# Kernel tuning notes

Hardware: AMD Instinct MI355X
Metric: run time of the kernel (lower is better)

## Reference

```python
import jax, jax.numpy as jnp
import numpy as np

N = 50000
E = 600000
F_IN = 128      # float features (in_channels - 1)
CE = 8          # cell embedding dim
D_IN = F_IN + CE  # 136
C = 128         # out_channels
NUM_CELLS = 854
NEG_SLOPE = 0.2
LN_EPS = 1e-5


def _gat_layer(x, src, dst, W, a_src, a_dst, b):
    """PyG GATConv, heads=1, concat=False, add_self_loops already in src/dst.
    x: [N, Din]; src/dst: [Etot]; W: [Din, C]; a_src/a_dst: [C]; b: [C].
    """
    h = x @ W                               # [N, C]
    alpha_src = h @ a_src                   # [N]
    alpha_dst = h @ a_dst                   # [N]
    e = jax.nn.leaky_relu(alpha_src[src] + alpha_dst[dst], NEG_SLOPE)  # [Etot]
    # segment softmax over edges sharing a destination node
    m = jax.ops.segment_max(e, dst, num_segments=N)    # [N] (every node has a self-loop)
    ex = jnp.exp(e - m[dst])                           # [Etot]
    denom = jax.ops.segment_sum(ex, dst, num_segments=N)  # [N]
    alpha = ex / denom[dst]                            # [Etot]
    out = jax.ops.segment_sum(h[src] * alpha[:, None], dst, num_segments=N)  # [N, C]
    return out + b


def _layer_norm(x, g, b):
    mu = jnp.mean(x, axis=-1, keepdims=True)
    var = jnp.var(x, axis=-1, keepdims=True)
    return (x - mu) * jax.lax.rsqrt(var + LN_EPS) * g + b


def setup_inputs() -> dict:
    key = jax.random.key(0)
    ks = jax.random.split(key, 12)
    x_base = jax.random.normal(ks[0], (N, F_IN), dtype=jnp.float32)
    cell_ids = jax.random.randint(ks[1], (N,), 0, NUM_CELLS, dtype=jnp.int64)
    edge_index = jax.random.randint(ks[2], (2, E), 0, N, dtype=jnp.int64)
    s = 0.05
    cell_emb = jax.random.normal(ks[3], (NUM_CELLS, CE), dtype=jnp.float32)
    W1 = jax.random.normal(ks[4], (D_IN, C), dtype=jnp.float32) * s
    a_src1 = jax.random.normal(ks[5], (C,), dtype=jnp.float32) * s
    a_dst1 = jax.random.normal(ks[6], (C,), dtype=jnp.float32) * s
    b1 = jnp.zeros((C,), dtype=jnp.float32)
    ln_g = jnp.ones((C,), dtype=jnp.float32)
    ln_b = jnp.zeros((C,), dtype=jnp.float32)
    W2 = jax.random.normal(ks[7], (C, C), dtype=jnp.float32) * s
    a_src2 = jax.random.normal(ks[8], (C,), dtype=jnp.float32) * s
    a_dst2 = jax.random.normal(ks[9], (C,), dtype=jnp.float32) * s
    b2 = jnp.zeros((C,), dtype=jnp.float32)
    return {
        "x_base": x_base, "cell_ids": cell_ids, "edge_index": edge_index,
        "cell_emb": cell_emb,
        "W1": W1, "a_src1": a_src1, "a_dst1": a_dst1, "b1": b1,
        "ln_g": ln_g, "ln_b": ln_b,
        "W2": W2, "a_src2": a_src2, "a_dst2": a_dst2, "b2": b2,
    }


def reference(x_base, cell_ids, edge_index, cell_emb,
              W1, a_src1, a_dst1, b1, ln_g, ln_b,
              W2, a_src2, a_dst2, b2):
    # embed cell ids and concat (equiv. to x[:, :-1] + Embedding(x[:, -1]))
    x = jnp.concatenate([x_base, cell_emb[cell_ids]], axis=1)   # [N, 136]
    # PyG GATConv adds self-loops internally
    loops = jnp.arange(N, dtype=edge_index.dtype)
    src = jnp.concatenate([edge_index[0], loops])
    dst = jnp.concatenate([edge_index[1], loops])
    # layer 1 + LN + ELU (dropout inactive in eval mode)
    x = _gat_layer(x, src, dst, W1, a_src1, a_dst1, b1)
    x = jax.nn.elu(_layer_norm(x, ln_g, ln_b))
    # layer 2 (no norm/activation on last layer)
    x = _gat_layer(x, src, dst, W2, a_src2, a_dst2, b2)
    return x
```

## Files before the change

### kernel.cpp

```cpp
#include <hip/hip_runtime.h>
#include <hip/hip_fp16.h>
#include <cstdint>
#include <cstddef>

#define NEG_SLOPE 0.2f
#define LN_EPS 1e-5f

constexpr int BS = 256;
constexpr int STRIDE = 96;

typedef _Float16 f16x8 __attribute__((ext_vector_type(8)));
typedef float f32x4 __attribute__((ext_vector_type(4)));

__global__ __launch_bounds__(256) void k_init(
    int* __restrict__ cnt, unsigned short* __restrict__ sn,
    const float* __restrict__ W1, const float* __restrict__ W2,
    _Float16* __restrict__ Wt1, _Float16* __restrict__ Wt2,
    int n, int nbN)
{
    int b = blockIdx.x;
    if (b < nbN) {
        int i = b * BS + threadIdx.x;
        if (i < n) { cnt[i] = 1; sn[(size_t)i * STRIDE] = (unsigned short)i; }
    } else {
        int idx = (b - nbN) * BS + threadIdx.x;
        if (idx < 128 * 160) {
            int nn = idx / 160, k = idx - nn * 160;
            Wt1[idx] = (_Float16)((k < 136) ? W1[(size_t)k * 128 + nn] : 0.f);
        } else if (idx < 128 * 160 + 128 * 128) {
            int j = idx - 128 * 160;
            int nn = j >> 7, k = j & 127;
            Wt2[j] = (_Float16)W2[(size_t)k * 128 + nn];
        }
    }
}

__global__ __launch_bounds__(256) void k_scatter_gemm1(
    const int* __restrict__ esrc, const int* __restrict__ edst,
    int* __restrict__ cnt, unsigned short* __restrict__ sn,
    const float* __restrict__ x, const int* __restrict__ cid,
    const float* __restrict__ emb,
    const _Float16* __restrict__ Wt1,
    const float* __restrict__ a_src, const float* __restrict__ a_dst,
    _Float16* __restrict__ hb, float* __restrict__ as_, float* __restrict__ ad_,
    int e, int n, int nbG, int nbA)
{
    __shared__ float red[2][16][2][2];
    int b = blockIdx.x;
    int role, idx;
    int nInter = 2 * (nbG < nbA ? nbG : nbA);
    if (b < nInter)      { role = b & 1; idx = b >> 1; }
    else if (nbG < nbA)  { role = 1; idx = (b - nInter) + nbG; }
    else                 { role = 0; idx = (b - nInter) + nbA; }

    if (role == 1) {
        int i = idx * BS + threadIdx.x;
        if (i < e) {
            int s = esrc[i], d = edst[i];
            int slot = atomicAdd(&cnt[d], 1);
            if (slot < STRIDE)
                sn[(size_t)d * STRIDE + slot] = (unsigned short)s;
        }
        return;
    }

    int tid = threadIdx.x;
    int wave = tid >> 6, lane = tid & 63;
    int rg = wave >> 1, ch = wave & 1;
    int r15 = lane & 15, q = lane >> 4;
    int rowBase = idx * 32 + rg * 16;
    int colBase = ch * 64;
    int row = rowBase + r15;
    bool ok = row < n;
    int rl = ok ? row : n - 1;

    f32x4 acc[4] = {};
    const _Float16* Wp[4];
    #pragma unroll
    for (int s = 0; s < 4; ++s)
        Wp[s] = Wt1 + (size_t)(colBase + s * 16 + r15) * 160 + q * 8;
    const float* Xp = x + (size_t)rl * 128 + q * 8;

    #pragma unroll
    for (int k0 = 0; k0 < 128; k0 += 32) {
        f16x8 wv[4];
        #pragma unroll
        for (int s = 0; s < 4; ++s) wv[s] = *(const f16x8*)(Wp[s] + k0);
        float4 xlo = *(const float4*)(Xp + k0);
        float4 xhi = *(const float4*)(Xp + k0 + 4);
        f16x8 xv;
        xv[0] = (_Float16)xlo.x; xv[1] = (_Float16)xlo.y;
        xv[2] = (_Float16)xlo.z; xv[3] = (_Float16)xlo.w;
        xv[4] = (_Float16)xhi.x; xv[5] = (_Float16)xhi.y;
        xv[6] = (_Float16)xhi.z; xv[7] = (_Float16)xhi.w;
        #pragma unroll
        for (int s = 0; s < 4; ++s)
            acc[s] = __builtin_amdgcn_mfma_f32_16x16x32_f16(wv[s], xv, acc[s], 0, 0, 0);
    }
    {
        f16x8 wv[4];
        #pragma unroll
        for (int s = 0; s < 4; ++s) wv[s] = *(const f16x8*)(Wp[s] + 128);
        f16x8 xv;
        #pragma unroll
        for (int j = 0; j < 8; ++j) xv[j] = (_Float16)0.f;
        if (q == 0) {
            const float* er = emb + (size_t)cid[rl] * 8;
            float4 e0 = *(const float4*)er;
            float4 e1 = *(const float4*)(er + 4);
            xv[0] = (_Float16)e0.x; xv[1] = (_Float16)e0.y;
            xv[2] = (_Float16)e0.z; xv[3] = (_Float16)e0.w;
            xv[4] = (_Float16)e1.x; xv[5] = (_Float16)e1.y;
            xv[6] = (_Float16)e1.z; xv[7] = (_Float16)e1.w;
        }
        #pragma unroll
        for (int s = 0; s < 4; ++s)
            acc[s] = __builtin_amdgcn_mfma_f32_16x16x32_f16(wv[s], xv, acc[s], 0, 0, 0);
    }

    float vs = 0.f, vd = 0.f;
    #pragma unroll
    for (int s = 0; s < 4; ++s) {
        float4 as4 = *(const float4*)&a_src[colBase + s * 16 + q * 4];
        float4 ad4 = *(const float4*)&a_dst[colBase + s * 16 + q * 4];
        f32x4 d = acc[s];
        vs += d[0]*as4.x + d[1]*as4.y + d[2]*as4.z + d[3]*as4.w;
        vd += d[0]*ad4.x + d[1]*ad4.y + d[2]*ad4.z + d[3]*ad4.w;
        if (ok) {
            ushort4 u;
            u.x = __half_as_ushort(__float2half_rn(d[0]));
            u.y = __half_as_ushort(__float2half_rn(d[1]));
            u.z = __half_as_ushort(__float2half_rn(d[2]));
            u.w = __half_as_ushort(__float2half_rn(d[3]));
            *(ushort4*)&hb[(size_t)row * 128 + colBase + s * 16 + q * 4] = u;
        }
    }
    vs += __shfl_xor(vs, 16); vs += __shfl_xor(vs, 32);
    vd += __shfl_xor(vd, 16); vd += __shfl_xor(vd, 32);
    if (q == 0) { red[rg][r15][ch][0] = vs; red[rg][r15][ch][1] = vd; }
    __syncthreads();
    if (ch == 0 && q == 0 && ok) {
        as_[row] = red[rg][r15][0][0] + red[rg][r15][1][0];
        ad_[row] = red[rg][r15][0][1] + red[rg][r15][1][1];
    }
}

__global__ __launch_bounds__(256) void k_agg1_gemm2(
    const _Float16* __restrict__ h1, const unsigned short* __restrict__ sn,
    const int* __restrict__ cnt, const float* __restrict__ as1,
    const float* __restrict__ ad1, const float* __restrict__ b1,
    const float* __restrict__ lng, const float* __restrict__ lnb,
    const _Float16* __restrict__ Wt2,
    const float* __restrict__ a_src2, const float* __restrict__ a_dst2,
    _Float16* __restrict__ h2, float* __restrict__ as2, float* __restrict__ ad2,
    int nn)
{
    __shared__ _Float16 yt[32][144];
    __shared__ float red[2][16][2][2];
    int t = blockIdx.x;
    int tid = threadIdx.x;
    int wave = tid >> 6, lane = tid & 63;
    int l4 = lane & 15, q = lane >> 4;
    const char* hbB = (const char*)h1;

    for (int i = 0; i < 8; ++i) {
        int node = t * 32 + wave * 8 + i;
        if (node >= nn) break;
        int len = cnt[node];
        len = len < STRIDE ? len : STRIDE;
        len = __builtin_amdgcn_readfirstlane(len);
        int start = node * STRIDE;
        float adv = ad1[node];

        float acc[8] = {0.f, 0.f, 0.f, 0.f, 0.f, 0.f, 0.f, 0.f};
        float dsum = 0.f;
        for (int j = 0; j < len; j += 16) {
            int rem = len - j;
            int offB = (l4 < rem) ? ((int)sn[start + j + l4] << 8) : 0;
            float tt = as1[offB >> 8] + adv;
            tt = tt > 0.f ? tt : NEG_SLOPE * tt;
            float w0 = __expf(fminf(tt, 70.f));
            #pragma unroll
            for (int v = 0; v < 4; ++v) {
                int e = 4 * v + q;
                int ob  = __shfl(offB, e);
                float w = __shfl(w0, e);
                if (e < rem) {
                    f16x8 hv = *(const f16x8*)(hbB + ob + l4 * 16);
                    #pragma unroll
                    for (int c = 0; c < 8; ++c)
                        acc[c] = fmaf(w, (float)hv[c], acc[c]);
                    dsum += w;
                }
            }
        }
        #pragma unroll
        for (int c = 0; c < 8; ++c) {
            acc[c] += __shfl_xor(acc[c], 16);
            acc[c] += __shfl_xor(acc[c], 32);
        }
        dsum += __shfl_xor(dsum, 16);
        dsum += __shfl_xor(dsum, 32);

        float inv = 1.f / dsum;
        float4 b0 = *(const float4*)&b1[l4 * 8];
        float4 bb = *(const float4*)&b1[l4 * 8 + 4];
        float vv[8];
        vv[0] = acc[0] * inv + b0.x; vv[1] = acc[1] * inv + b0.y;
        vv[2] = acc[2] * inv + b0.z; vv[3] = acc[3] * inv + b0.w;
        vv[4] = acc[4] * inv + bb.x; vv[5] = acc[5] * inv + bb.y;
        vv[6] = acc[6] * inv + bb.z; vv[7] = acc[7] * inv + bb.w;

        float s1 = 0.f, s2 = 0.f;
        #pragma unroll
        for (int c = 0; c < 8; ++c) { s1 += vv[c]; s2 += vv[c] * vv[c]; }
        #pragma unroll
        for (int o = 1; o < 16; o <<= 1) {
            s1 += __shfl_xor(s1, o);
            s2 += __shfl_xor(s2, o);
        }
        float mean = s1 * (1.f / 128.f);
        float var  = s2 * (1.f / 128.f) - mean * mean;
        float r = rsqrtf(var + LN_EPS);
        float4 g0 = *(const float4*)&lng[l4 * 8];
        float4 g1 = *(const float4*)&lng[l4 * 8 + 4];
        float4 p0 = *(const float4*)&lnb[l4 * 8];
        float4 p1 = *(const float4*)&lnb[l4 * 8 + 4];
        float gg[8] = {g0.x, g0.y, g0.z, g0.w, g1.x, g1.y, g1.z, g1.w};
        float pp[8] = {p0.x, p0.y, p0.z, p0.w, p1.x, p1.y, p1.z, p1.w};
        #pragma unroll
        for (int c = 0; c < 8; ++c) {
            float u = (vv[c] - mean) * r * gg[c] + pp[c];
            vv[c] = u > 0.f ? u : __expf(u) - 1.f;
        }

        if (q == 0) {
            f16x8 o;
            #pragma unroll
            for (int c = 0; c < 8; ++c) o[c] = (_Float16)vv[c];
            *(f16x8*)&yt[wave * 8 + i][l4 * 8] = o;
        }
    }
    __syncthreads();

    int rg = wave >> 1, ch = wave & 1;
    int r15 = lane & 15;
    int rowBase = t * 32 + rg * 16;
    int colBase = ch * 64;
    int row = rowBase + r15;
    bool ok = row < nn;

    f32x4 acc2[4] = {};
    const _Float16* Wp[4];
    #pragma unroll
    for (int s = 0; s < 4; ++s)
        Wp[s] = Wt2 + (size_t)(colBase + s * 16 + r15) * 128 + q * 8;
    const _Float16* Yp = &yt[rg * 16 + r15][q * 8];

    #pragma unroll
    for (int k0 = 0; k0 < 128; k0 += 32) {
        f16x8 wv[4];
        #pragma unroll
        for (int s = 0; s < 4; ++s) wv[s] = *(const f16x8*)(Wp[s] + k0);
        f16x8 xv = *(const f16x8*)(Yp + k0);
        #pragma unroll
        for (int s = 0; s < 4; ++s)
            acc2[s] = __builtin_amdgcn_mfma_f32_16x16x32_f16(wv[s], xv, acc2[s], 0, 0, 0);
    }

    float vs = 0.f, vd = 0.f;
    #pragma unroll
    for (int s = 0; s < 4; ++s) {
        float4 as4 = *(const float4*)&a_src2[colBase + s * 16 + q * 4];
        float4 ad4 = *(const float4*)&a_dst2[colBase + s * 16 + q * 4];
        f32x4 d = acc2[s];
        vs += d[0]*as4.x + d[1]*as4.y + d[2]*as4.z + d[3]*as4.w;
        vd += d[0]*ad4.x + d[1]*ad4.y + d[2]*ad4.z + d[3]*ad4.w;
        if (ok) {
            ushort4 u;
            u.x = __half_as_ushort(__float2half_rn(d[0]));
            u.y = __half_as_ushort(__float2half_rn(d[1]));
            u.z = __half_as_ushort(__float2half_rn(d[2]));
            u.w = __half_as_ushort(__float2half_rn(d[3]));
            *(ushort4*)&h2[(size_t)row * 128 + colBase + s * 16 + q * 4] = u;
        }
    }
    vs += __shfl_xor(vs, 16); vs += __shfl_xor(vs, 32);
    vd += __shfl_xor(vd, 16); vd += __shfl_xor(vd, 32);
    if (q == 0) { red[rg][r15][ch][0] = vs; red[rg][r15][ch][1] = vd; }
    __syncthreads();
    if (ch == 0 && q == 0 && ok) {
        as2[row] = red[rg][r15][0][0] + red[rg][r15][1][0];
        ad2[row] = red[rg][r15][0][1] + red[rg][r15][1][1];
    }
}

__global__ __launch_bounds__(256) void k_agg2(
    const _Float16* __restrict__ hb, const unsigned short* __restrict__ sn,
    const int* __restrict__ cnt, const float* __restrict__ as_,
    const float* __restrict__ ad_, const float* __restrict__ bias,
    float* __restrict__ out, int n_nodes)
{
    int wave = threadIdx.x >> 6, lane = threadIdx.x & 63;
    int n = blockIdx.x * 4 + wave;
    if (n >= n_nodes) return;
    int len = cnt[n];
    len = len < STRIDE ? len : STRIDE;
    len = __builtin_amdgcn_readfirstlane(len);
    int start = n * STRIDE;
    int l4 = lane & 15, q = lane >> 4;
    float adv = ad_[n];
    const char* hbB = (const char*)hb;

    float acc[8] = {0.f, 0.f, 0.f, 0.f, 0.f, 0.f, 0.f, 0.f};
    float dsum = 0.f;
    for (int j = 0; j < len; j += 16) {
        int rem = len - j;
        int offB = (l4 < rem) ? ((int)sn[start + j + l4] << 8) : 0;
        float t = as_[offB >> 8] + adv;
        t = t > 0.f ? t : NEG_SLOPE * t;
        float w0 = __expf(fminf(t, 70.f));
        #pragma unroll
        for (int v = 0; v < 4; ++v) {
            int e = 4 * v + q;
            int ob  = __shfl(offB, e);
            float w = __shfl(w0, e);
            if (e < rem) {
                f16x8 hv = *(const f16x8*)(hbB + ob + l4 * 16);
                #pragma unroll
                for (int c = 0; c < 8; ++c)
                    acc[c] = fmaf(w, (float)hv[c], acc[c]);
                dsum += w;
            }
        }
    }
    #pragma unroll
    for (int c = 0; c < 8; ++c) {
        acc[c] += __shfl_xor(acc[c], 16);
        acc[c] += __shfl_xor(acc[c], 32);
    }
    dsum += __shfl_xor(dsum, 16);
    dsum += __shfl_xor(dsum, 32);

    if (q == 0) {
        float inv = 1.f / dsum;
        float4 b0 = *(const float4*)&bias[l4 * 8];
        float4 b1 = *(const float4*)&bias[l4 * 8 + 4];
        float4 o0 = make_float4(acc[0]*inv + b0.x, acc[1]*inv + b0.y,
                                acc[2]*inv + b0.z, acc[3]*inv + b0.w);
        float4 o1 = make_float4(acc[4]*inv + b1.x, acc[5]*inv + b1.y,
                                acc[6]*inv + b1.z, acc[7]*inv + b1.w);
        *(float4*)(out + (size_t)n * 128 + l4 * 8)     = o0;
        *(float4*)(out + (size_t)n * 128 + l4 * 8 + 4) = o1;
    }
}


extern "C" void kernel_launch(void* const* d_in, const int* in_sizes, int n_in,
                              void* d_out, int out_size, void* d_ws, size_t ws_size,
                              hipStream_t stream) {
    const float* x_base   = (const float*)d_in[0];
    const int*   cell_ids = (const int*)d_in[1];
    const int*   eidx     = (const int*)d_in[2];
    const float* cell_emb = (const float*)d_in[3];
    const float* W1     = (const float*)d_in[4];
    const float* a_src1 = (const float*)d_in[5];
    const float* a_dst1 = (const float*)d_in[6];
    const float* b1     = (const float*)d_in[7];
    const float* ln_g   = (const float*)d_in[8];
    const float* ln_b   = (const float*)d_in[9];
    const float* W2     = (const float*)d_in[10];
    const float* a_src2 = (const float*)d_in[11];
    const float* a_dst2 = (const float*)d_in[12];
    const float* b2     = (const float*)d_in[13];

    const int N = in_sizes[0] / 128;
    const int E = in_sizes[2] / 2;

    const int* esrc = eidx;
    const int* edst = eidx + E;

    auto align = [](size_t v) { return (v + 255) & ~(size_t)255; };
    char* p = (char*)d_ws;
    int*   cnt    = (int*)p;   p += align((size_t)N * 4);
    unsigned short* sn = (unsigned short*)p; p += align((size_t)N * STRIDE * 2 + 64);
    _Float16* h1  = (_Float16*)p; p += align((size_t)N * 128 * 2);
    _Float16* h2  = (_Float16*)p; p += align((size_t)N * 128 * 2);
    _Float16* Wt1 = (_Float16*)p; p += align((size_t)128 * 160 * 2);
    _Float16* Wt2 = (_Float16*)p; p += align((size_t)128 * 128 * 2);
    float* as1    = (float*)p; p += align((size_t)N * 4);
    float* ad1    = (float*)p; p += align((size_t)N * 4);
    float* as2    = (float*)p; p += align((size_t)N * 4);
    float* ad2    = (float*)p; p += align((size_t)N * 4);
    (void)ws_size; (void)n_in; (void)out_size;

    const int nbN = (N + BS - 1) / BS;
    const int nbA = (E + BS - 1) / BS;
    const int nbG = (N + 31) / 32;
    const int wblocks = (128 * 160 + 128 * 128 + BS - 1) / BS;

    k_init<<<nbN + wblocks, BS, 0, stream>>>(cnt, sn, W1, W2, Wt1, Wt2, N, nbN);
    k_scatter_gemm1<<<nbG + nbA, BS, 0, stream>>>(
        esrc, edst, cnt, sn, x_base, cell_ids, cell_emb, Wt1,
        a_src1, a_dst1, h1, as1, ad1, E, N, nbG, nbA);
    k_agg1_gemm2<<<nbG, BS, 0, stream>>>(
        h1, sn, cnt, as1, ad1, b1, ln_g, ln_b, Wt2,
        a_src2, a_dst2, h2, as2, ad2, N);
    k_agg2<<<(N + 3) / 4, BS, 0, stream>>>(
        h2, sn, cnt, as2, ad2, b2, (float*)d_out, N);
}
```

Before: 242.1 us.

## Assign one node per quarter-wave in aggregation kernels and widen GEMM2 block

Both aggregation kernels now process one destination node per 16-lane group instead of one per wave. Each group reads four neighbor indices with a single 8-byte load and walks edges four at a time, which removes the cross-quarter shuffle reductions and cuts idle lanes for low-degree nodes. The fused agg1+GEMM2 kernel moves to 512-thread blocks so all 32 nodes of a tile aggregate in parallel, and it splits the MFMA output columns across four waves. The 8-byte index loads may read unset slots past the node's neighbor count; those values are used to index as1/as2 without a bounds check.

```diff
diff --git a/kernel.cpp b/kernel.cpp
--- a/kernel.cpp
+++ b/kernel.cpp
@@ -145,7 +145,7 @@
     }
 }
 
-__global__ __launch_bounds__(256) void k_agg1_gemm2(
+__global__ __launch_bounds__(512, 8) void k_agg1_gemm2(
     const _Float16* __restrict__ h1, const unsigned short* __restrict__ sn,
     const int* __restrict__ cnt, const float* __restrict__ as1,
     const float* __restrict__ ad1, const float* __restrict__ b1,
@@ -156,52 +156,49 @@
     int nn)
 {
     __shared__ _Float16 yt[32][144];
-    __shared__ float red[2][16][2][2];
+    __shared__ float red[2][16][4][2];
     int t = blockIdx.x;
     int tid = threadIdx.x;
     int wave = tid >> 6, lane = tid & 63;
     int l4 = lane & 15, q = lane >> 4;
+    int qg = wave * 4 + q;
+    int node = t * 32 + qg;
+    bool valid = node < nn;
     const char* hbB = (const char*)h1;
 
-    for (int i = 0; i < 8; ++i) {
-        int node = t * 32 + wave * 8 + i;
-        if (node >= nn) break;
-        int len = cnt[node];
+    int len = 0; float adv = 0.f;
+    if (valid) {
+        len = cnt[node];
         len = len < STRIDE ? len : STRIDE;
-        len = __builtin_amdgcn_readfirstlane(len);
-        int start = node * STRIDE;
-        float adv = ad1[node];
-
-        float acc[8] = {0.f, 0.f, 0.f, 0.f, 0.f, 0.f, 0.f, 0.f};
-        float dsum = 0.f;
-        for (int j = 0; j < len; j += 16) {
-            int rem = len - j;
-            int offB = (l4 < rem) ? ((int)sn[start + j + l4] << 8) : 0;
-            float tt = as1[offB >> 8] + adv;
-            tt = tt > 0.f ? tt : NEG_SLOPE * tt;
-            float w0 = __expf(fminf(tt, 70.f));
-            #pragma unroll
-            for (int v = 0; v < 4; ++v) {
-                int e = 4 * v + q;
-                int ob  = __shfl(offB, e);
-                float w = __shfl(w0, e);
-                if (e < rem) {
-                    f16x8 hv = *(const f16x8*)(hbB + ob + l4 * 16);
-                    #pragma unroll
-                    for (int c = 0; c < 8; ++c)
-                        acc[c] = fmaf(w, (float)hv[c], acc[c]);
-                    dsum += w;
-                }
+        adv = ad1[node];
+    }
+    int start = node * STRIDE;
+    int sub = l4 & 3;
+
+    float acc[8] = {0.f, 0.f, 0.f, 0.f, 0.f, 0.f, 0.f, 0.f};
+    float dsum = 0.f;
+    for (int j = 0; j < len; j += 4) {
+        int rem = len - j;
+        unsigned long long s4 = *(const unsigned long long*)(sn + start + j);
+        int my = (int)((s4 >> (sub * 16)) & 0xFFFFull);
+        float tt = as1[my] + adv;
+        tt = tt > 0.f ? tt : NEG_SLOPE * tt;
+        float w = __expf(fminf(tt, 70.f));
+        #pragma unroll
+        for (int i = 0; i < 4; ++i) {
+            if (i < rem) {
+                int si = (int)((s4 >> (i * 16)) & 0xFFFFull);
+                float wi = __shfl(w, (lane & 48) | i);
+                f16x8 hv = *(const f16x8*)(hbB + ((size_t)si << 8) + l4 * 16);
+                #pragma unroll
+                for (int c = 0; c < 8; ++c)
+                    acc[c] = fmaf(wi, (float)hv[c], acc[c]);
+                dsum += wi;
             }
         }
-        #pragma unroll
-        for (int c = 0; c < 8; ++c) {
-            acc[c] += __shfl_xor(acc[c], 16);
-            acc[c] += __shfl_xor(acc[c], 32);
-        }
-        dsum += __shfl_xor(dsum, 16);
-        dsum += __shfl_xor(dsum, 32);
-
+    }
+
+    if (valid) {
         float inv = 1.f / dsum;
         float4 b0 = *(const float4*)&b1[l4 * 8];
         float4 bb = *(const float4*)&b1[l4 * 8 + 4];
@@ -228,51 +225,50 @@
         float4 p1 = *(const float4*)&lnb[l4 * 8 + 4];
         float gg[8] = {g0.x, g0.y, g0.z, g0.w, g1.x, g1.y, g1.z, g1.w};
         float pp[8] = {p0.x, p0.y, p0.z, p0.w, p1.x, p1.y, p1.z, p1.w};
+        f16x8 o;
         #pragma unroll
         for (int c = 0; c < 8; ++c) {
             float u = (vv[c] - mean) * r * gg[c] + pp[c];
-            vv[c] = u > 0.f ? u : __expf(u) - 1.f;
-        }
-
-        if (q == 0) {
-            f16x8 o;
-            #pragma unroll
-            for (int c = 0; c < 8; ++c) o[c] = (_Float16)vv[c];
-            *(f16x8*)&yt[wave * 8 + i][l4 * 8] = o;
-        }
+            u = u > 0.f ? u : __expf(u) - 1.f;
+            o[c] = (_Float16)u;
+        }
+        *(f16x8*)&yt[qg][l4 * 8] = o;
+    } else {
+        f16x8 z;
+        #pragma unroll
+        for (int c = 0; c < 8; ++c) z[c] = (_Float16)0.f;
+        *(f16x8*)&yt[qg][l4 * 8] = z;
     }
     __syncthreads();
 
-    int rg = wave >> 1, ch = wave & 1;
-    int r15 = lane & 15;
-    int rowBase = t * 32 + rg * 16;
-    int colBase = ch * 64;
-    int row = rowBase + r15;
+    int rg = wave >> 2, cc = wave & 3;
+    int r15 = l4;
+    int row = t * 32 + rg * 16 + r15;
     bool ok = row < nn;
 
-    f32x4 acc2[4] = {};
-    const _Float16* Wp[4];
-    #pragma unroll
-    for (int s = 0; s < 4; ++s)
-        Wp[s] = Wt2 + (size_t)(colBase + s * 16 + r15) * 128 + q * 8;
+    f32x4 acc2[2] = {};
+    const _Float16* Wp[2];
+    #pragma unroll
+    for (int s = 0; s < 2; ++s)
+        Wp[s] = Wt2 + (size_t)(cc * 32 + s * 16 + r15) * 128 + q * 8;
     const _Float16* Yp = &yt[rg * 16 + r15][q * 8];
 
     #pragma unroll
     for (int k0 = 0; k0 < 128; k0 += 32) {
-        f16x8 wv[4];
-        #pragma unroll
-        for (int s = 0; s < 4; ++s) wv[s] = *(const f16x8*)(Wp[s] + k0);
+        f16x8 wv[2];
+        #pragma unroll
+        for (int s = 0; s < 2; ++s) wv[s] = *(const f16x8*)(Wp[s] + k0);
         f16x8 xv = *(const f16x8*)(Yp + k0);
         #pragma unroll
-        for (int s = 0; s < 4; ++s)
+        for (int s = 0; s < 2; ++s)
             acc2[s] = __builtin_amdgcn_mfma_f32_16x16x32_f16(wv[s], xv, acc2[s], 0, 0, 0);
     }
 
     float vs = 0.f, vd = 0.f;
     #pragma unroll
-    for (int s = 0; s < 4; ++s) {
-        float4 as4 = *(const float4*)&a_src2[colBase + s * 16 + q * 4];
-        float4 ad4 = *(const float4*)&a_dst2[colBase + s * 16 + q * 4];
+    for (int s = 0; s < 2; ++s) {
+        float4 as4 = *(const float4*)&a_src2[cc * 32 + s * 16 + q * 4];
+        float4 ad4 = *(const float4*)&a_dst2[cc * 32 + s * 16 + q * 4];
         f32x4 d = acc2[s];
         vs += d[0]*as4.x + d[1]*as4.y + d[2]*as4.z + d[3]*as4.w;
         vd += d[0]*ad4.x + d[1]*ad4.y + d[2]*ad4.z + d[3]*ad4.w;
@@ -282,16 +278,18 @@
             u.y = __half_as_ushort(__float2half_rn(d[1]));
             u.z = __half_as_ushort(__float2half_rn(d[2]));
             u.w = __half_as_ushort(__float2half_rn(d[3]));
-            *(ushort4*)&h2[(size_t)row * 128 + colBase + s * 16 + q * 4] = u;
+            *(ushort4*)&h2[(size_t)row * 128 + cc * 32 + s * 16 + q * 4] = u;
         }
     }
     vs += __shfl_xor(vs, 16); vs += __shfl_xor(vs, 32);
     vd += __shfl_xor(vd, 16); vd += __shfl_xor(vd, 32);
-    if (q == 0) { red[rg][r15][ch][0] = vs; red[rg][r15][ch][1] = vd; }
+    if (q == 0) { red[rg][r15][cc][0] = vs; red[rg][r15][cc][1] = vd; }
     __syncthreads();
-    if (ch == 0 && q == 0 && ok) {
-        as2[row] = red[rg][r15][0][0] + red[rg][r15][1][0];
-        ad2[row] = red[rg][r15][0][1] + red[rg][r15][1][1];
+    if (cc == 0 && q == 0 && ok) {
+        as2[row] = red[rg][r15][0][0] + red[rg][r15][1][0]
+                 + red[rg][r15][2][0] + red[rg][r15][3][0];
+        ad2[row] = red[rg][r15][0][1] + red[rg][r15][1][1]
+                 + red[rg][r15][2][1] + red[rg][r15][3][1];
     }
 }
 
@@ -301,58 +299,50 @@
     const float* __restrict__ ad_, const float* __restrict__ bias,
     float* __restrict__ out, int n_nodes)
 {
-    int wave = threadIdx.x >> 6, lane = threadIdx.x & 63;
-    int n = blockIdx.x * 4 + wave;
-    if (n >= n_nodes) return;
-    int len = cnt[n];
+    int tid = threadIdx.x;
+    int wave = tid >> 6, lane = tid & 63;
+    int l4 = lane & 15, q = lane >> 4;
+    int node = blockIdx.x * 16 + wave * 4 + q;
+    if (node >= n_nodes) return;
+    int len = cnt[node];
     len = len < STRIDE ? len : STRIDE;
-    len = __builtin_amdgcn_readfirstlane(len);
-    int start = n * STRIDE;
-    int l4 = lane & 15, q = lane >> 4;
-    float adv = ad_[n];
+    int start = node * STRIDE;
+    int sub = l4 & 3;
+    float adv = ad_[node];
     const char* hbB = (const char*)hb;
 
     float acc[8] = {0.f, 0.f, 0.f, 0.f, 0.f, 0.f, 0.f, 0.f};
     float dsum = 0.f;
-    for (int j = 0; j < len; j += 16) {
+    for (int j = 0; j < len; j += 4) {
         int rem = len - j;
-        int offB = (l4 < rem) ? ((int)sn[start + j + l4] << 8) : 0;
-        float t = as_[offB >> 8] + adv;
+        unsigned long long s4 = *(const unsigned long long*)(sn + start + j);
+        int my = (int)((s4 >> (sub * 16)) & 0xFFFFull);
+        float t = as_[my] + adv;
         t = t > 0.f ? t : NEG_SLOPE * t;
-        float w0 = __expf(fminf(t, 70.f));
-        #pragma unroll
-        for (int v = 0; v < 4; ++v) {
-            int e = 4 * v + q;
-            int ob  = __shfl(offB, e);
-            float w = __shfl(w0, e);
-            if (e < rem) {
-                f16x8 hv = *(const f16x8*)(hbB + ob + l4 * 16);
+        float w = __expf(fminf(t, 70.f));
+        #pragma unroll
+        for (int i = 0; i < 4; ++i) {
+            if (i < rem) {
+                int si = (int)((s4 >> (i * 16)) & 0xFFFFull);
+                float wi = __shfl(w, (lane & 48) | i);
+                f16x8 hv = *(const f16x8*)(hbB + ((size_t)si << 8) + l4 * 16);
                 #pragma unroll
                 for (int c = 0; c < 8; ++c)
-                    acc[c] = fmaf(w, (float)hv[c], acc[c]);
-                dsum += w;
+                    acc[c] = fmaf(wi, (float)hv[c], acc[c]);
+                dsum += wi;
             }
         }
     }
-    #pragma unroll
-    for (int c = 0; c < 8; ++c) {
-        acc[c] += __shfl_xor(acc[c], 16);
-        acc[c] += __shfl_xor(acc[c], 32);
-    }
-    dsum += __shfl_xor(dsum, 16);
-    dsum += __shfl_xor(dsum, 32);
-
-    if (q == 0) {
-        float inv = 1.f / dsum;
-        float4 b0 = *(const float4*)&bias[l4 * 8];
-        float4 b1 = *(const float4*)&bias[l4 * 8 + 4];
-        float4 o0 = make_float4(acc[0]*inv + b0.x, acc[1]*inv + b0.y,
-                                acc[2]*inv + b0.z, acc[3]*inv + b0.w);
-        float4 o1 = make_float4(acc[4]*inv + b1.x, acc[5]*inv + b1.y,
-                                acc[6]*inv + b1.z, acc[7]*inv + b1.w);
-        *(float4*)(out + (size_t)n * 128 + l4 * 8)     = o0;
-        *(float4*)(out + (size_t)n * 128 + l4 * 8 + 4) = o1;
-    }
+
+    float inv = 1.f / dsum;
+    float4 b0 = *(const float4*)&bias[l4 * 8];
+    float4 b1 = *(const float4*)&bias[l4 * 8 + 4];
+    float4 o0 = make_float4(acc[0]*inv + b0.x, acc[1]*inv + b0.y,
+                            acc[2]*inv + b0.z, acc[3]*inv + b0.w);
+    float4 o1 = make_float4(acc[4]*inv + b1.x, acc[5]*inv + b1.y,
+                            acc[6]*inv + b1.z, acc[7]*inv + b1.w);
+    *(float4*)(out + (size_t)node * 128 + l4 * 8)     = o0;
+    *(float4*)(out + (size_t)node * 128 + l4 * 8 + 4) = o1;
 }
 
 
@@ -403,9 +393,9 @@
     k_scatter_gemm1<<<nbG + nbA, BS, 0, stream>>>(
         esrc, edst, cnt, sn, x_base, cell_ids, cell_emb, Wt1,
         a_src1, a_dst1, h1, as1, ad1, E, N, nbG, nbA);
-    k_agg1_gemm2<<<nbG, BS, 0, stream>>>(
+    k_agg1_gemm2<<<nbG, 512, 0, stream>>>(
         h1, sn, cnt, as1, ad1, b1, ln_g, ln_b, Wt2,
         a_src2, a_dst2, h2, as2, ad2, N);
-    k_agg2<<<(N + 3) / 4, BS, 0, stream>>>(
+    k_agg2<<<(N + 15) / 16, BS, 0, stream>>>(
         h2, sn, cnt, as2, ad2, b2, (float*)d_out, N);
 }
```

After: 221.0 us. 1.1x faster.
